# Kernel optimization log

Measured on AMD Instinct MI355X. Metric: run time of the kernel, lower is better.

Reference implementation:

```python
import jax, jax.numpy as jnp
import numpy as np

N = 2048      # total nodes across all graphs
G = 16        # number of graphs
IN = 16       # input_dim
D = 256       # hidden_dim (d_model)
NH = 8        # num_heads
HD = D // NH  # head_dim
FF = 4 * D    # dim_feedforward
L = 4         # num_layers
LAT = 32      # latent_dim
BH = D // 2   # beta_head hidden
LN_EPS = 1e-5


def setup_inputs() -> dict:
    key = jax.random.key(0)
    ks = jax.random.split(key, 32)

    def w(k, shape, fan_in):
        return jax.random.normal(k, shape, jnp.float32) * (1.0 / np.sqrt(fan_in))

    inp = {
        "x": jax.random.normal(ks[0], (N, IN), jnp.float32),
        "coords": jax.random.normal(ks[1], (N, 3), jnp.float32),
        "batch": jnp.sort(jax.random.randint(ks[2], (N,), 0, G)).astype(jnp.int32),
        # input projection
        "Wi": w(ks[3], (IN, D), IN), "bi": jnp.zeros((D,), jnp.float32),
        # per-layer transformer params, stacked on leading layer dim
        "qkv_w": w(ks[4], (L, D, 3 * D), D), "qkv_b": jnp.zeros((L, 3 * D), jnp.float32),
        "out_w": w(ks[5], (L, D, D), D),     "out_b": jnp.zeros((L, D), jnp.float32),
        "ff1_w": w(ks[6], (L, D, FF), D),    "ff1_b": jnp.zeros((L, FF), jnp.float32),
        "ff2_w": w(ks[7], (L, FF, D), FF),   "ff2_b": jnp.zeros((L, D), jnp.float32),
        "ln1_s": jnp.ones((L, D), jnp.float32), "ln1_b": jnp.zeros((L, D), jnp.float32),
        "ln2_s": jnp.ones((L, D), jnp.float32), "ln2_b": jnp.zeros((L, D), jnp.float32),
        # heads
        "lat_w": w(ks[8], (D, LAT), D), "lat_b": jnp.zeros((LAT,), jnp.float32),
        "b1_w": w(ks[9], (D, BH), D),   "b1_b": jnp.zeros((BH,), jnp.float32),
        "b2_w": w(ks[10], (BH, 1), BH), "b2_b": jnp.zeros((1,), jnp.float32),
    }
    return inp


def _layer_norm(h, s, b):
    m = jnp.mean(h, axis=-1, keepdims=True)
    v = jnp.mean(jnp.square(h - m), axis=-1, keepdims=True)
    return (h - m) * jax.lax.rsqrt(v + LN_EPS) * s + b


def _forward(x, batch, Wi, bi, qkv_w, qkv_b, out_w, out_b, ff1_w, ff1_b,
             ff2_w, ff2_b, ln1_s, ln1_b, ln2_s, ln2_b, lat_w, lat_b,
             b1_w, b1_b, b2_w, b2_b):
    n = x.shape[0]
    h = x @ Wi + bi  # [N, D]
    # the per-graph python loop in torch == block-diagonal attention mask
    attn_bias = jnp.where(batch[:, None] == batch[None, :], 0.0, -1e9).astype(h.dtype)  # [N, N]
    scale = 1.0 / np.sqrt(HD)
    for l in range(L):
        qkv = h @ qkv_w[l] + qkv_b[l]                 # [N, 3D]
        q, k, v = jnp.split(qkv, 3, axis=-1)
        q = q.reshape(n, NH, HD)
        k = k.reshape(n, NH, HD)
        v = v.reshape(n, NH, HD)
        scores = jnp.einsum('nhd,mhd->hnm', q, k) * scale + attn_bias[None]  # [H, N, N]
        a = jax.nn.softmax(scores, axis=-1)
        o = jnp.einsum('hnm,mhd->nhd', a, v).reshape(n, D)
        o = o @ out_w[l] + out_b[l]
        h = _layer_norm(h + o, ln1_s[l], ln1_b[l])     # post-norm (torch default)
        f = jax.nn.relu(h @ ff1_w[l] + ff1_b[l]) @ ff2_w[l] + ff2_b[l]
        h = _layer_norm(h + f, ln2_s[l], ln2_b[l])
    lat = h @ lat_w + lat_b                            # [N, LAT]
    norm = jnp.maximum(jnp.linalg.norm(lat, axis=-1, keepdims=True), 1e-12)
    lat = lat / norm * np.sqrt(LAT)
    beta = jax.nn.sigmoid(jax.nn.relu(h @ b1_w + b1_b) @ b2_w + b2_b)  # [N, 1]
    beta = jnp.clip(beta, 1e-6, 1.0 - 1e-6)
    return beta, lat


def reference(x, coords, batch, Wi, bi, qkv_w, qkv_b, out_w, out_b,
              ff1_w, ff1_b, ff2_w, ff2_b, ln1_s, ln1_b, ln2_s, ln2_b,
              lat_w, lat_b, b1_w, b1_b, b2_w, b2_b):
    # coords is accepted (signature fidelity) but unused in the original forward
    del coords
    return _forward(x, batch, Wi, bi, qkv_w, qkv_b, out_w, out_b, ff1_w, ff1_b,
                    ff2_w, ff2_b, ln1_s, ln1_b, ln2_s, ln2_b, lat_w, lat_b,
                    b1_w, b1_b, b2_w, b2_b)
```

## Files before the change

### kernel.cpp

```cpp
#include <hip/hip_runtime.h>
#include <hip/hip_bf16.h>

typedef __attribute__((ext_vector_type(8))) short bf16x8;
typedef __attribute__((ext_vector_type(4))) float f32x4;

__device__ inline float wave_sum64(float v) {
#pragma unroll
  for (int m = 32; m >= 1; m >>= 1) v += __shfl_xor(v, m, 64);
  return v;
}
__device__ inline ushort f2bf(float f) {
  uint u = __float_as_uint(f);
  return (ushort)((u + 0x7FFFu + ((u >> 16) & 1u)) >> 16);
}

__global__ __launch_bounds__(256) void pack_weights(
    const float* __restrict__ qkv_w, const float* __restrict__ out_w,
    const float* __restrict__ ff1_w, const float* __restrict__ ff2_w,
    const float* __restrict__ b1_w, const float* __restrict__ lat_w,
    short* __restrict__ qkv_t, short* __restrict__ out_t,
    short* __restrict__ ff1_t, short* __restrict__ ff2_t,
    short* __restrict__ b1_t, short* __restrict__ lat_t,
    const int* __restrict__ batch, int* __restrict__ starts, int* __restrict__ meta) {
  int t = blockIdx.x;
  if (t == 3112) {
    for (int i = threadIdx.x; i < 2048; i += 256) {
      int b = batch[i];
      if (i == 0) {
        for (int g = 0; g <= b; ++g) starts[g] = 0;
      } else {
        int bp = batch[i - 1];
        for (int g = bp + 1; g <= b; ++g) starts[g] = i;
      }
      if (i == 2047) {
        for (int g = b + 1; g <= 16; ++g) starts[g] = 2048;
      }
    }
    __syncthreads();
    if (threadIdx.x == 0) {
      int nt = 0;
      for (int g = 0; g < 16; ++g) {
        const int js = starts[g], je = starts[g + 1];
        for (int q0 = js; q0 < je; q0 += 16) {
          meta[1 + nt * 3] = q0;
          meta[2 + nt * 3] = js;
          meta[3 + nt * 3] = je;
          ++nt;
        }
      }
      meta[0] = nt;
    }
    return;
  }
  const float* src;
  short* dst;
  int Kd, Nd, rem;
  if (t < 768) {
    int l = t / 192; rem = t % 192; Kd = 256; Nd = 768;
    src = qkv_w + (size_t)l * Kd * Nd; dst = qkv_t + (size_t)l * Nd * Kd;
  } else if (t < 1024) {
    t -= 768; int l = t / 64; rem = t % 64; Kd = 256; Nd = 256;
    src = out_w + (size_t)l * Kd * Nd; dst = out_t + (size_t)l * Nd * Kd;
  } else if (t < 2048) {
    t -= 1024; int l = t / 256; rem = t % 256; Kd = 256; Nd = 1024;
    src = ff1_w + (size_t)l * Kd * Nd; dst = ff1_t + (size_t)l * Nd * Kd;
  } else if (t < 3072) {
    t -= 2048; int l = t / 256; rem = t % 256; Kd = 1024; Nd = 256;
    src = ff2_w + (size_t)l * Kd * Nd; dst = ff2_t + (size_t)l * Nd * Kd;
  } else if (t < 3104) {
    rem = t - 3072; Kd = 256; Nd = 128; src = b1_w; dst = b1_t;
  } else {
    rem = t - 3104; Kd = 256; Nd = 32; src = lat_w; dst = lat_t;
  }
  const int ntn = Nd / 32;
  const int kt = rem / ntn, nt = rem % ntn;

  __shared__ float tile[32][33];
  const int tx = threadIdx.x & 31, ty = threadIdx.x >> 5;
#pragma unroll
  for (int r = 0; r < 4; ++r) {
    int k = kt * 32 + ty + r * 8;
    tile[ty + r * 8][tx] = src[(size_t)k * Nd + nt * 32 + tx];
  }
  __syncthreads();
#pragma unroll
  for (int r = 0; r < 4; ++r) {
    int n = nt * 32 + ty + r * 8;
    dst[(size_t)n * Kd + kt * 32 + tx] = (short)f2bf(tile[tx][ty + r * 8]);
  }
}

__global__ __launch_bounds__(256) void inproj_kernel(
    const float* __restrict__ x, const float* __restrict__ Wi,
    const float* __restrict__ bi, float* __restrict__ h, short* __restrict__ hb) {
  __shared__ float xs[16];
  const int i = blockIdx.x, j = threadIdx.x;
  if (j < 16) xs[j] = x[(size_t)i * 16 + j];
  __syncthreads();
  float acc = bi[j];
#pragma unroll
  for (int k = 0; k < 16; ++k) acc += xs[k] * Wi[k * 256 + j];
  h[(size_t)i * 256 + j] = acc;
  hb[(size_t)i * 256 + j] = (short)f2bf(acc);
}

template <int ACT, int OUTBF, int VT>
__global__ __launch_bounds__(256) void gemm_bf16(
    const short* __restrict__ A, const short* __restrict__ Bt,
    const float* __restrict__ bias, float* __restrict__ Cf, short* __restrict__ Cb,
    short* __restrict__ vtg, int M, int N, int K, int kpb) {
  __shared__ short As[64 * 128];
  __shared__ short Bs[64 * 128];

  const int t = threadIdx.x;
  const int bm = blockIdx.y, bn = blockIdx.x, bz = blockIdx.z;
  const int srow = t >> 2, sq = t & 3;
  const int lane = t & 63, wid = t >> 6;
  const int wr = wid >> 1, wc = wid & 1;
  const int fr = lane & 15, fs = lane >> 4;
  const int rx = srow & 7;

  f32x4 acc[2][2];
#pragma unroll
  for (int m = 0; m < 2; ++m)
#pragma unroll
    for (int n = 0; n < 2; ++n) acc[m][n] = (f32x4){0.f, 0.f, 0.f, 0.f};

  const int kbase = bz * kpb;
  const short* ap = A + (size_t)(bm * 64 + srow) * K + kbase;
  const int ng = bn * 64 + srow;
  const short* bp = Bt + (size_t)ng * K + kbase;

  const int ar0 = wr * 32 + fr, ar1 = ar0 + 16;
  const int bc0 = wc * 32 + fr, bc1 = bc0 + 16;

  for (int k0 = 0; k0 < kpb; k0 += 128) {
    bf16x8 av[4], bv[4];
#pragma unroll
    for (int i = 0; i < 4; ++i) av[i] = *(const bf16x8*)(ap + k0 + (sq * 4 + i) * 8);
    if (ng < N) {
#pragma unroll
      for (int i = 0; i < 4; ++i) bv[i] = *(const bf16x8*)(bp + k0 + (sq * 4 + i) * 8);
    } else {
#pragma unroll
      for (int i = 0; i < 4; ++i) bv[i] = (bf16x8){0, 0, 0, 0, 0, 0, 0, 0};
    }
    __syncthreads();
#pragma unroll
    for (int i = 0; i < 4; ++i) {
      const int s = sq * 4 + i;
      *(bf16x8*)(As + srow * 128 + ((s ^ rx) * 8)) = av[i];
      *(bf16x8*)(Bs + srow * 128 + ((s ^ rx) * 8)) = bv[i];
    }
    __syncthreads();

#pragma unroll
    for (int ks = 0; ks < 4; ++ks) {
      const int u = ks * 4 + fs;
      bf16x8 a0 = *(const bf16x8*)(As + ar0 * 128 + ((u ^ (ar0 & 7)) * 8));
      bf16x8 a1 = *(const bf16x8*)(As + ar1 * 128 + ((u ^ (ar1 & 7)) * 8));
      bf16x8 b0 = *(const bf16x8*)(Bs + bc0 * 128 + ((u ^ (bc0 & 7)) * 8));
      bf16x8 b1 = *(const bf16x8*)(Bs + bc1 * 128 + ((u ^ (bc1 & 7)) * 8));
      acc[0][0] = __builtin_amdgcn_mfma_f32_16x16x32_bf16(a0, b0, acc[0][0], 0, 0, 0);
      acc[0][1] = __builtin_amdgcn_mfma_f32_16x16x32_bf16(a0, b1, acc[0][1], 0, 0, 0);
      acc[1][0] = __builtin_amdgcn_mfma_f32_16x16x32_bf16(a1, b0, acc[1][0], 0, 0, 0);
      acc[1][1] = __builtin_amdgcn_mfma_f32_16x16x32_bf16(a1, b1, acc[1][1], 0, 0, 0);
    }
  }

#pragma unroll
  for (int n = 0; n < 2; ++n) {
    const int col = bn * 64 + wc * 32 + n * 16 + fr;
    if (col >= N) continue;
    const float bvv = (bz == 0) ? bias[col] : 0.f;
#pragma unroll
    for (int m = 0; m < 2; ++m) {
      const int rbase = bm * 64 + wr * 32 + m * 16 + fs * 4;
#pragma unroll
      for (int j = 0; j < 4; ++j) {
        float v = acc[m][n][j] + bvv;
        if (ACT == 1) v = fmaxf(v, 0.f);
        if (OUTBF) {
          const short bfv = (short)f2bf(v);
          Cb[(size_t)(rbase + j) * N + col] = bfv;
          if (VT && col >= 512) {
            vtg[(size_t)(col - 512) * 2048 + rbase + j] = bfv;
          }
        } else {
          Cf[(size_t)(bz * M + rbase + j) * N + col] = v;
        }
      }
    }
  }
}

__global__ __launch_bounds__(256) void attn_direct(
    const short* __restrict__ qkv, const short* __restrict__ vtg,
    const int* __restrict__ meta, short* __restrict__ out) {
  const int wid = blockIdx.x * 4 + (threadIdx.x >> 6);
  const int tile = wid >> 3, h = wid & 7;
  if (tile >= meta[0]) return;
  const int lane = threadIdx.x & 63;
  const int fr = lane & 15, fs = lane >> 4;
  const int q0 = meta[1 + tile * 3];
  const int js = meta[2 + tile * 3];
  const int je = meta[3 + tile * 3];
  const int jbase = js & ~15;
  const int njt = (je - jbase + 15) >> 4;
  const float scale = 0.17677669529663687f;

  const int qrow = min(q0 + fr, 2047);
  const bf16x8 qf = *(const bf16x8*)(qkv + (size_t)qrow * 768 + h * 32 + fs * 8);
  const int jeq = (q0 + fr < je) ? je : 0;

  f32x4 s[16];
#pragma unroll
  for (int jt = 0; jt < 16; ++jt)
    s[jt] = (f32x4){-3.0e38f, -3.0e38f, -3.0e38f, -3.0e38f};

#pragma unroll
  for (int jt = 0; jt < 16; ++jt) {
    if (jt < njt) {
      const int krow = min(jbase + jt * 16 + fr, 2047);
      const bf16x8 kf = *(const bf16x8*)(qkv + (size_t)krow * 768 + 256 + h * 32 + fs * 8);
      s[jt] = __builtin_amdgcn_mfma_f32_16x16x32_bf16(
          kf, qf, (f32x4){0.f, 0.f, 0.f, 0.f}, 0, 0, 0);
    }
  }
  float mx = -3.0e38f;
#pragma unroll
  for (int jt = 0; jt < 16; ++jt) {
    if (jt < njt) {
#pragma unroll
      for (int jj = 0; jj < 4; ++jj) {
        const int j = jbase + jt * 16 + fs * 4 + jj;
        const bool valid = (j >= js) && (j < jeq);
        s[jt][jj] = valid ? s[jt][jj] * scale : -3.0e38f;
        mx = fmaxf(mx, s[jt][jj]);
      }
    }
  }
  mx = fmaxf(mx, __shfl_xor(mx, 16, 64));
  mx = fmaxf(mx, __shfl_xor(mx, 32, 64));
  float l = 0.f;
#pragma unroll
  for (int jt = 0; jt < 16; ++jt) {
#pragma unroll
    for (int jj = 0; jj < 4; ++jj) {
      const float p = __expf(s[jt][jj] - mx);
      s[jt][jj] = p;
      l += p;
    }
  }
  l += __shfl_xor(l, 16, 64);
  l += __shfl_xor(l, 32, 64);

  f32x4 oa[2];
  oa[0] = (f32x4){0.f, 0.f, 0.f, 0.f};
  oa[1] = (f32x4){0.f, 0.f, 0.f, 0.f};
#pragma unroll
  for (int p2 = 0; p2 < 8; ++p2) {
    if (p2 * 2 < njt) {
      bf16x8 pa;
      pa[0] = (short)f2bf(s[p2 * 2][0]);     pa[1] = (short)f2bf(s[p2 * 2][1]);
      pa[2] = (short)f2bf(s[p2 * 2][2]);     pa[3] = (short)f2bf(s[p2 * 2][3]);
      pa[4] = (short)f2bf(s[p2 * 2 + 1][0]); pa[5] = (short)f2bf(s[p2 * 2 + 1][1]);
      pa[6] = (short)f2bf(s[p2 * 2 + 1][2]); pa[7] = (short)f2bf(s[p2 * 2 + 1][3]);
      const int jb0 = min(jbase + p2 * 32 + fs * 4, 2044);
      const int jb1 = min(jbase + p2 * 32 + 16 + fs * 4, 2044);
#pragma unroll
      for (int nt = 0; nt < 2; ++nt) {
        const short* vrow = vtg + (size_t)(h * 32 + nt * 16 + fr) * 2048;
        const short4 v0 = *(const short4*)(vrow + jb0);
        const short4 v1 = *(const short4*)(vrow + jb1);
        bf16x8 vf;
        vf[0] = v0.x; vf[1] = v0.y; vf[2] = v0.z; vf[3] = v0.w;
        vf[4] = v1.x; vf[5] = v1.y; vf[6] = v1.z; vf[7] = v1.w;
        oa[nt] = __builtin_amdgcn_mfma_f32_16x16x32_bf16(pa, vf, oa[nt], 0, 0, 0);
      }
    }
  }

#pragma unroll
  for (int jj = 0; jj < 4; ++jj) {
    const float lq = __shfl(l, fs * 4 + jj, 64);
    const int node = q0 + fs * 4 + jj;
    if (node < je) {
      const float inv = 1.f / lq;
      out[(size_t)node * 256 + h * 32 + fr] = (short)f2bf(oa[0][jj] * inv);
      out[(size_t)node * 256 + h * 32 + 16 + fr] = (short)f2bf(oa[1][jj] * inv);
    }
  }
}

template <int P>
__global__ __launch_bounds__(256) void ln_kernel(
    const float* __restrict__ base, const float* __restrict__ delta,
    const float* __restrict__ s, const float* __restrict__ b,
    float* __restrict__ outf, short* __restrict__ outb) {
  const int row = blockIdx.x * 4 + (threadIdx.x >> 6);
  const int lane = threadIdx.x & 63;
  const float4 xa = *(const float4*)(base + (size_t)row * 256 + lane * 4);
  float4 v = xa;
#pragma unroll
  for (int p = 0; p < P; ++p) {
    const float4 xb = *(const float4*)(delta + (size_t)(p * 2048 + row) * 256 + lane * 4);
    v.x += xb.x; v.y += xb.y; v.z += xb.z; v.w += xb.w;
  }
  float sum = v.x + v.y + v.z + v.w;
  sum = wave_sum64(sum);
  const float mean = sum * (1.f / 256.f);
  float4 d = make_float4(v.x - mean, v.y - mean, v.z - mean, v.w - mean);
  float sq = d.x * d.x + d.y * d.y + d.z * d.z + d.w * d.w;
  sq = wave_sum64(sq);
  const float rs = rsqrtf(sq * (1.f / 256.f) + 1e-5f);
  const float4 sv = *(const float4*)(s + lane * 4);
  const float4 bv = *(const float4*)(b + lane * 4);
  float4 o = make_float4(d.x * rs * sv.x + bv.x, d.y * rs * sv.y + bv.y,
                         d.z * rs * sv.z + bv.z, d.w * rs * sv.w + bv.w);
  *(float4*)(outf + (size_t)row * 256 + lane * 4) = o;
  short4 ob;
  ob.x = (short)f2bf(o.x); ob.y = (short)f2bf(o.y);
  ob.z = (short)f2bf(o.z); ob.w = (short)f2bf(o.w);
  *(short4*)(outb + (size_t)row * 256 + lane * 4) = ob;
}

__global__ __launch_bounds__(256) void lat_kernel(
    const short* __restrict__ A, const short* __restrict__ Bt,
    const float* __restrict__ bias, float* __restrict__ out) {
  __shared__ short As[64 * 128];
  __shared__ short Bs[64 * 128];
  const int t = threadIdx.x;
  const int bm = blockIdx.x;
  const int srow = t >> 2, sq = t & 3;
  const int lane = t & 63, w = t >> 6;
  const int fr = lane & 15, fs = lane >> 4;
  const int rx = srow & 7;

  f32x4 acc[2];
  acc[0] = (f32x4){0.f, 0.f, 0.f, 0.f};
  acc[1] = (f32x4){0.f, 0.f, 0.f, 0.f};

  const short* ap = A + (size_t)(bm * 64 + srow) * 256;
  const short* bp = Bt + (size_t)srow * 256;
  const int ar = w * 16 + fr;

  for (int k0 = 0; k0 < 256; k0 += 128) {
    bf16x8 av[4], bv[4];
#pragma unroll
    for (int i = 0; i < 4; ++i) av[i] = *(const bf16x8*)(ap + k0 + (sq * 4 + i) * 8);
    if (srow < 32) {
#pragma unroll
      for (int i = 0; i < 4; ++i) bv[i] = *(const bf16x8*)(bp + k0 + (sq * 4 + i) * 8);
    } else {
#pragma unroll
      for (int i = 0; i < 4; ++i) bv[i] = (bf16x8){0, 0, 0, 0, 0, 0, 0, 0};
    }
    __syncthreads();
#pragma unroll
    for (int i = 0; i < 4; ++i) {
      const int s = sq * 4 + i;
      *(bf16x8*)(As + srow * 128 + ((s ^ rx) * 8)) = av[i];
      *(bf16x8*)(Bs + srow * 128 + ((s ^ rx) * 8)) = bv[i];
    }
    __syncthreads();
#pragma unroll
    for (int ks = 0; ks < 4; ++ks) {
      const int u = ks * 4 + fs;
      bf16x8 a0 = *(const bf16x8*)(As + ar * 128 + ((u ^ (ar & 7)) * 8));
      bf16x8 b0 = *(const bf16x8*)(Bs + fr * 128 + ((u ^ (fr & 7)) * 8));
      bf16x8 b1 = *(const bf16x8*)(Bs + (16 + fr) * 128 + ((u ^ ((16 + fr) & 7)) * 8));
      acc[0] = __builtin_amdgcn_mfma_f32_16x16x32_bf16(a0, b0, acc[0], 0, 0, 0);
      acc[1] = __builtin_amdgcn_mfma_f32_16x16x32_bf16(a0, b1, acc[1], 0, 0, 0);
    }
  }

  const float b0v = bias[fr], b1v = bias[16 + fr];
#pragma unroll
  for (int j = 0; j < 4; ++j) {
    const int row = bm * 64 + w * 16 + fs * 4 + j;
    float v0 = acc[0][j] + b0v;
    float v1 = acc[1][j] + b1v;
    float ss = v0 * v0 + v1 * v1;
    ss += __shfl_xor(ss, 1, 64);
    ss += __shfl_xor(ss, 2, 64);
    ss += __shfl_xor(ss, 4, 64);
    ss += __shfl_xor(ss, 8, 64);
    const float inv = 5.656854249492381f / fmaxf(sqrtf(ss), 1e-12f);
    out[(size_t)row * 32 + fr] = v0 * inv;
    out[(size_t)row * 32 + 16 + fr] = v1 * inv;
  }
}

__global__ __launch_bounds__(256) void beta_kernel(
    const float* __restrict__ bh, const float* __restrict__ w,
    const float* __restrict__ b2b, float* __restrict__ beta) {
  const int row = blockIdx.x * 4 + (threadIdx.x >> 6);
  const int lane = threadIdx.x & 63;
  float p = bh[(size_t)row * 128 + lane] * w[lane] +
            bh[(size_t)row * 128 + 64 + lane] * w[64 + lane];
  p = wave_sum64(p);
  if (lane == 0) {
    float x = p + b2b[0];
    float sgm = 1.f / (1.f + __expf(-x));
    sgm = fminf(fmaxf(sgm, 1e-6f), 1.f - 1e-6f);
    beta[row] = sgm;
  }
}

extern "C" void kernel_launch(void* const* d_in, const int* in_sizes, int n_in,
                              void* d_out, int out_size, void* d_ws, size_t ws_size,
                              hipStream_t stream) {
  const int N = 2048, D = 256, FF = 1024, L = 4;

  const float* x     = (const float*)d_in[0];
  const int*   batch = (const int*)d_in[2];
  const float* Wi    = (const float*)d_in[3];
  const float* bi    = (const float*)d_in[4];
  const float* qkv_w = (const float*)d_in[5];
  const float* qkv_b = (const float*)d_in[6];
  const float* out_w = (const float*)d_in[7];
  const float* out_b = (const float*)d_in[8];
  const float* ff1_w = (const float*)d_in[9];
  const float* ff1_b = (const float*)d_in[10];
  const float* ff2_w = (const float*)d_in[11];
  const float* ff2_b = (const float*)d_in[12];
  const float* ln1_s = (const float*)d_in[13];
  const float* ln1_b = (const float*)d_in[14];
  const float* ln2_s = (const float*)d_in[15];
  const float* ln2_b = (const float*)d_in[16];
  const float* lat_w = (const float*)d_in[17];
  const float* lat_b = (const float*)d_in[18];
  const float* b1_w  = (const float*)d_in[19];
  const float* b1_b  = (const float*)d_in[20];
  const float* b2_w  = (const float*)d_in[21];
  const float* b2_b  = (const float*)d_in[22];

  float* ws = (float*)d_ws;
  float* h      = ws;
  float* tmp    = h + (size_t)N * D;
  float* bh     = tmp + (size_t)4 * N * D;
  int*  starts  = (int*)(bh + (size_t)N * 128);
  int*  meta    = starts + 32;
  short* hb     = (short*)(meta + 448);
  short* qkvb   = hb + (size_t)N * D;
  short* attnb  = qkvb + (size_t)N * 3 * D;
  short* ffb    = attnb + (size_t)N * D;
  short* vtg    = ffb + (size_t)N * FF;
  short* qkv_t  = vtg + (size_t)256 * 2048;
  short* out_t  = qkv_t + (size_t)L * 768 * 256;
  short* ff1_t  = out_t + (size_t)L * 256 * 256;
  short* ff2_t  = ff1_t + (size_t)L * 1024 * 256;
  short* b1_t   = ff2_t + (size_t)L * 256 * 1024;
  short* lat_t  = b1_t + (size_t)128 * 256;

  float* beta_out = (float*)d_out;
  float* lat_out  = beta_out + N;

  pack_weights<<<3113, 256, 0, stream>>>(qkv_w, out_w, ff1_w, ff2_w, b1_w, lat_w,
                                         qkv_t, out_t, ff1_t, ff2_t, b1_t, lat_t,
                                         batch, starts, meta);
  inproj_kernel<<<N, 256, 0, stream>>>(x, Wi, bi, h, hb);

  for (int l = 0; l < L; ++l) {
    gemm_bf16<0, 1, 1><<<dim3(12, 32, 1), 256, 0, stream>>>(
        hb, qkv_t + (size_t)l * 768 * 256, qkv_b + (size_t)l * 768,
        nullptr, qkvb, vtg, N, 768, 256, 256);
    attn_direct<<<288, 256, 0, stream>>>(qkvb, vtg, meta, attnb);
    gemm_bf16<0, 0, 0><<<dim3(4, 32, 2), 256, 0, stream>>>(
        attnb, out_t + (size_t)l * 256 * 256, out_b + (size_t)l * 256,
        tmp, nullptr, nullptr, N, 256, 256, 128);
    ln_kernel<2><<<N / 4, 256, 0, stream>>>(h, tmp, ln1_s + (size_t)l * D,
                                            ln1_b + (size_t)l * D, h, hb);
    gemm_bf16<1, 1, 0><<<dim3(16, 32, 1), 256, 0, stream>>>(
        hb, ff1_t + (size_t)l * FF * 256, ff1_b + (size_t)l * FF,
        nullptr, ffb, nullptr, N, FF, 256, 256);
    gemm_bf16<0, 0, 0><<<dim3(4, 32, 4), 256, 0, stream>>>(
        ffb, ff2_t + (size_t)l * 256 * FF, ff2_b + (size_t)l * 256,
        tmp, nullptr, nullptr, N, 256, 1024, 256);
    ln_kernel<4><<<N / 4, 256, 0, stream>>>(h, tmp, ln2_s + (size_t)l * D,
                                            ln2_b + (size_t)l * D, h, hb);
  }

  lat_kernel<<<N / 64, 256, 0, stream>>>(hb, lat_t, lat_b, lat_out);
  gemm_bf16<1, 0, 0><<<dim3(2, 32, 1), 256, 0, stream>>>(
      hb, b1_t, b1_b, bh, nullptr, nullptr, N, 128, 256, 256);
  beta_kernel<<<N / 4, 256, 0, stream>>>(bh, b2_w, b2_b, beta_out);
}
```

Baseline: 220.1 us.

## Fuse out-proj/FF2 GEMMs with residual LayerNorm and beta head, tile V transpose

Replaces the split-K fp32 GEMMs plus separate LayerNorm kernels with a single gemm_ln kernel per sublayer. Each block computes 16 full rows of 256 columns, adds bias and residual, and normalizes in-register with a shared-memory reduction. The beta head's two-stage GEMM and dot product become one fused kernel, and the V transpose write in the QKV GEMM now goes through LDS for coalesced stores. This removes the fp32 partial-sum traffic and several launches per layer. The cost is that gemm_ln runs only 128 blocks with no LDS staging or split-K, so the K=1024 FF2 path may have little parallelism, and variance is now computed as E[x²]−mean².

Result: slower. 320.5 us (+45.6%).

```diff
diff --git a/kernel.cpp b/kernel.cpp
--- a/kernel.cpp
+++ b/kernel.cpp
@@ -4,11 +4,6 @@
 typedef __attribute__((ext_vector_type(8))) short bf16x8;
 typedef __attribute__((ext_vector_type(4))) float f32x4;
 
-__device__ inline float wave_sum64(float v) {
-#pragma unroll
-  for (int m = 32; m >= 1; m >>= 1) v += __shfl_xor(v, m, 64);
-  return v;
-}
 __device__ inline ushort f2bf(float f) {
   uint u = __float_as_uint(f);
   return (ushort)((u + 0x7FFFu + ((u >> 16) & 1u)) >> 16);
@@ -104,16 +99,16 @@
   hb[(size_t)i * 256 + j] = (short)f2bf(acc);
 }
 
-template <int ACT, int OUTBF, int VT>
+template <int ACT, int VT>
 __global__ __launch_bounds__(256) void gemm_bf16(
     const short* __restrict__ A, const short* __restrict__ Bt,
-    const float* __restrict__ bias, float* __restrict__ Cf, short* __restrict__ Cb,
-    short* __restrict__ vtg, int M, int N, int K, int kpb) {
+    const float* __restrict__ bias, short* __restrict__ Cb,
+    short* __restrict__ vtg, int N, int K) {
   __shared__ short As[64 * 128];
   __shared__ short Bs[64 * 128];
 
   const int t = threadIdx.x;
-  const int bm = blockIdx.y, bn = blockIdx.x, bz = blockIdx.z;
+  const int bm = blockIdx.y, bn = blockIdx.x;
   const int srow = t >> 2, sq = t & 3;
   const int lane = t & 63, wid = t >> 6;
   const int wr = wid >> 1, wc = wid & 1;
@@ -126,15 +121,13 @@
 #pragma unroll
     for (int n = 0; n < 2; ++n) acc[m][n] = (f32x4){0.f, 0.f, 0.f, 0.f};
 
-  const int kbase = bz * kpb;
-  const short* ap = A + (size_t)(bm * 64 + srow) * K + kbase;
+  const short* ap = A + (size_t)(bm * 64 + srow) * K;
   const int ng = bn * 64 + srow;
-  const short* bp = Bt + (size_t)ng * K + kbase;
-
+  const short* bp = Bt + (size_t)ng * K;
   const int ar0 = wr * 32 + fr, ar1 = ar0 + 16;
   const int bc0 = wc * 32 + fr, bc1 = bc0 + 16;
 
-  for (int k0 = 0; k0 < kpb; k0 += 128) {
+  for (int k0 = 0; k0 < K; k0 += 128) {
     bf16x8 av[4], bv[4];
 #pragma unroll
     for (int i = 0; i < 4; ++i) av[i] = *(const bf16x8*)(ap + k0 + (sq * 4 + i) * 8);
@@ -153,7 +146,6 @@
       *(bf16x8*)(Bs + srow * 128 + ((s ^ rx) * 8)) = bv[i];
     }
     __syncthreads();
-
 #pragma unroll
     for (int ks = 0; ks < 4; ++ks) {
       const int u = ks * 4 + fs;
@@ -171,25 +163,43 @@
 #pragma unroll
   for (int n = 0; n < 2; ++n) {
     const int col = bn * 64 + wc * 32 + n * 16 + fr;
-    if (col >= N) continue;
-    const float bvv = (bz == 0) ? bias[col] : 0.f;
-#pragma unroll
-    for (int m = 0; m < 2; ++m) {
-      const int rbase = bm * 64 + wr * 32 + m * 16 + fs * 4;
-#pragma unroll
-      for (int j = 0; j < 4; ++j) {
-        float v = acc[m][n][j] + bvv;
-        if (ACT == 1) v = fmaxf(v, 0.f);
-        if (OUTBF) {
-          const short bfv = (short)f2bf(v);
-          Cb[(size_t)(rbase + j) * N + col] = bfv;
-          if (VT && col >= 512) {
-            vtg[(size_t)(col - 512) * 2048 + rbase + j] = bfv;
-          }
-        } else {
-          Cf[(size_t)(bz * M + rbase + j) * N + col] = v;
+    if (col < N) {
+      const float bvv = bias[col];
+#pragma unroll
+      for (int m = 0; m < 2; ++m) {
+        const int rbase = bm * 64 + wr * 32 + m * 16 + fs * 4;
+#pragma unroll
+        for (int j = 0; j < 4; ++j) {
+          float v = acc[m][n][j] + bvv;
+          if (ACT == 1) v = fmaxf(v, 0.f);
+          Cb[(size_t)(rbase + j) * N + col] = (short)f2bf(v);
         }
       }
+    }
+  }
+
+  if (VT && bn >= 8) {
+    short* tr = As;
+    __syncthreads();
+#pragma unroll
+    for (int n = 0; n < 2; ++n) {
+      const int c = wc * 32 + n * 16 + fr;
+      const float bvv = bias[bn * 64 + c];
+#pragma unroll
+      for (int m = 0; m < 2; ++m)
+#pragma unroll
+        for (int j = 0; j < 4; ++j) {
+          const int r = wr * 32 + m * 16 + fs * 4 + j;
+          tr[c * 68 + r] = (short)f2bf(acc[m][n][j] + bvv);
+        }
+    }
+    __syncthreads();
+    const int tx = t & 63, ty = t >> 6;
+    const int d0 = bn * 64 - 512, rb = bm * 64;
+#pragma unroll
+    for (int r = 0; r < 16; ++r) {
+      const int d = ty * 16 + r;
+      vtg[(size_t)(d0 + d) * 2048 + rb + tx] = tr[d * 68 + tx];
     }
   }
 }
@@ -280,7 +290,6 @@
       }
     }
   }
-
 #pragma unroll
   for (int jj = 0; jj < 4; ++jj) {
     const float lq = __shfl(l, fs * 4 + jj, 64);
@@ -293,36 +302,123 @@
   }
 }
 
-template <int P>
-__global__ __launch_bounds__(256) void ln_kernel(
-    const float* __restrict__ base, const float* __restrict__ delta,
-    const float* __restrict__ s, const float* __restrict__ b,
-    float* __restrict__ outf, short* __restrict__ outb) {
-  const int row = blockIdx.x * 4 + (threadIdx.x >> 6);
-  const int lane = threadIdx.x & 63;
-  const float4 xa = *(const float4*)(base + (size_t)row * 256 + lane * 4);
-  float4 v = xa;
-#pragma unroll
-  for (int p = 0; p < P; ++p) {
-    const float4 xb = *(const float4*)(delta + (size_t)(p * 2048 + row) * 256 + lane * 4);
-    v.x += xb.x; v.y += xb.y; v.z += xb.z; v.w += xb.w;
-  }
-  float sum = v.x + v.y + v.z + v.w;
-  sum = wave_sum64(sum);
-  const float mean = sum * (1.f / 256.f);
-  float4 d = make_float4(v.x - mean, v.y - mean, v.z - mean, v.w - mean);
-  float sq = d.x * d.x + d.y * d.y + d.z * d.z + d.w * d.w;
-  sq = wave_sum64(sq);
-  const float rs = rsqrtf(sq * (1.f / 256.f) + 1e-5f);
-  const float4 sv = *(const float4*)(s + lane * 4);
-  const float4 bv = *(const float4*)(b + lane * 4);
-  float4 o = make_float4(d.x * rs * sv.x + bv.x, d.y * rs * sv.y + bv.y,
-                         d.z * rs * sv.z + bv.z, d.w * rs * sv.w + bv.w);
-  *(float4*)(outf + (size_t)row * 256 + lane * 4) = o;
-  short4 ob;
-  ob.x = (short)f2bf(o.x); ob.y = (short)f2bf(o.y);
-  ob.z = (short)f2bf(o.z); ob.w = (short)f2bf(o.w);
-  *(short4*)(outb + (size_t)row * 256 + lane * 4) = ob;
+__global__ __launch_bounds__(256) void gemm_ln(
+    const short* __restrict__ A, const short* __restrict__ Bt,
+    const float* __restrict__ bias, const float* __restrict__ lns,
+    const float* __restrict__ lnb, float* __restrict__ hio,
+    short* __restrict__ hbo, int K) {
+  __shared__ float red[128];
+  const int t = threadIdx.x, lane = t & 63, w = t >> 6;
+  const int fr = lane & 15, fs = lane >> 4;
+  const int rb = blockIdx.x * 16;
+
+  f32x4 acc[4];
+#pragma unroll
+  for (int n = 0; n < 4; ++n) acc[n] = (f32x4){0.f, 0.f, 0.f, 0.f};
+  const short* ap = A + (size_t)(rb + fr) * K;
+  const short* bp = Bt + (size_t)(w * 64 + fr) * K;
+  for (int k0 = 0; k0 < K; k0 += 32) {
+    const bf16x8 af = *(const bf16x8*)(ap + k0 + fs * 8);
+#pragma unroll
+    for (int n = 0; n < 4; ++n) {
+      const bf16x8 bf = *(const bf16x8*)(bp + (size_t)n * 16 * K + k0 + fs * 8);
+      acc[n] = __builtin_amdgcn_mfma_f32_16x16x32_bf16(af, bf, acc[n], 0, 0, 0);
+    }
+  }
+
+  float d[4][4];
+#pragma unroll
+  for (int n = 0; n < 4; ++n) {
+    const int col = w * 64 + n * 16 + fr;
+    const float bv = bias[col];
+#pragma unroll
+    for (int j = 0; j < 4; ++j) {
+      const int row = rb + fs * 4 + j;
+      d[n][j] = acc[n][j] + bv + hio[(size_t)row * 256 + col];
+    }
+  }
+  float ps[4], pq[4];
+#pragma unroll
+  for (int j = 0; j < 4; ++j) {
+    ps[j] = d[0][j] + d[1][j] + d[2][j] + d[3][j];
+    pq[j] = d[0][j] * d[0][j] + d[1][j] * d[1][j] + d[2][j] * d[2][j] + d[3][j] * d[3][j];
+#pragma unroll
+    for (int m = 1; m <= 8; m <<= 1) {
+      ps[j] += __shfl_xor(ps[j], m, 64);
+      pq[j] += __shfl_xor(pq[j], m, 64);
+    }
+  }
+  if (fr == 0) {
+#pragma unroll
+    for (int j = 0; j < 4; ++j) {
+      red[w * 16 + fs * 4 + j] = ps[j];
+      red[64 + w * 16 + fs * 4 + j] = pq[j];
+    }
+  }
+  __syncthreads();
+#pragma unroll
+  for (int j = 0; j < 4; ++j) {
+    const int row = fs * 4 + j;
+    const float S = red[row] + red[16 + row] + red[32 + row] + red[48 + row];
+    const float Q = red[64 + row] + red[80 + row] + red[96 + row] + red[112 + row];
+    const float mean = S * (1.f / 256.f);
+    const float var = Q * (1.f / 256.f) - mean * mean;
+    const float rs = rsqrtf(var + 1e-5f);
+#pragma unroll
+    for (int n = 0; n < 4; ++n) {
+      const int col = w * 64 + n * 16 + fr;
+      const float o = (d[n][j] - mean) * rs * lns[col] + lnb[col];
+      hio[(size_t)(rb + row) * 256 + col] = o;
+      hbo[(size_t)(rb + row) * 256 + col] = (short)f2bf(o);
+    }
+  }
+}
+
+__global__ __launch_bounds__(256) void gemm_beta(
+    const short* __restrict__ A, const short* __restrict__ Bt,
+    const float* __restrict__ b1b, const float* __restrict__ w2,
+    const float* __restrict__ b2b, float* __restrict__ beta) {
+  __shared__ float red[64];
+  const int t = threadIdx.x, lane = t & 63, w = t >> 6;
+  const int fr = lane & 15, fs = lane >> 4;
+  const int rb = blockIdx.x * 16;
+
+  f32x4 acc[2];
+  acc[0] = (f32x4){0.f, 0.f, 0.f, 0.f};
+  acc[1] = (f32x4){0.f, 0.f, 0.f, 0.f};
+  const short* ap = A + (size_t)(rb + fr) * 256;
+  const short* bp = Bt + (size_t)(w * 32 + fr) * 256;
+  for (int k0 = 0; k0 < 256; k0 += 32) {
+    const bf16x8 af = *(const bf16x8*)(ap + k0 + fs * 8);
+#pragma unroll
+    for (int n = 0; n < 2; ++n) {
+      const bf16x8 bf = *(const bf16x8*)(bp + (size_t)n * 16 * 256 + k0 + fs * 8);
+      acc[n] = __builtin_amdgcn_mfma_f32_16x16x32_bf16(af, bf, acc[n], 0, 0, 0);
+    }
+  }
+  const int c0 = w * 32 + fr, c1 = c0 + 16;
+  const float b0 = b1b[c0], b1 = b1b[c1];
+  const float w0 = w2[c0], w1 = w2[c1];
+  float part[4];
+#pragma unroll
+  for (int j = 0; j < 4; ++j) {
+    const float d0 = fmaxf(acc[0][j] + b0, 0.f);
+    const float d1 = fmaxf(acc[1][j] + b1, 0.f);
+    part[j] = d0 * w0 + d1 * w1;
+#pragma unroll
+    for (int m = 1; m <= 8; m <<= 1) part[j] += __shfl_xor(part[j], m, 64);
+  }
+  if (fr == 0) {
+#pragma unroll
+    for (int j = 0; j < 4; ++j) red[w * 16 + fs * 4 + j] = part[j];
+  }
+  __syncthreads();
+  if (t < 16) {
+    const float S = red[t] + red[16 + t] + red[32 + t] + red[48 + t] + b2b[0];
+    float sgm = 1.f / (1.f + __expf(-S));
+    sgm = fminf(fmaxf(sgm, 1e-6f), 1.f - 1e-6f);
+    beta[rb + t] = sgm;
+  }
 }
 
 __global__ __launch_bounds__(256) void lat_kernel(
@@ -340,7 +436,6 @@
   f32x4 acc[2];
   acc[0] = (f32x4){0.f, 0.f, 0.f, 0.f};
   acc[1] = (f32x4){0.f, 0.f, 0.f, 0.f};
-
   const short* ap = A + (size_t)(bm * 64 + srow) * 256;
   const short* bp = Bt + (size_t)srow * 256;
   const int ar = w * 16 + fr;
@@ -374,7 +469,6 @@
       acc[1] = __builtin_amdgcn_mfma_f32_16x16x32_bf16(a0, b1, acc[1], 0, 0, 0);
     }
   }
-
   const float b0v = bias[fr], b1v = bias[16 + fr];
 #pragma unroll
   for (int j = 0; j < 4; ++j) {
@@ -389,22 +483,6 @@
     const float inv = 5.656854249492381f / fmaxf(sqrtf(ss), 1e-12f);
     out[(size_t)row * 32 + fr] = v0 * inv;
     out[(size_t)row * 32 + 16 + fr] = v1 * inv;
-  }
-}
-
-__global__ __launch_bounds__(256) void beta_kernel(
-    const float* __restrict__ bh, const float* __restrict__ w,
-    const float* __restrict__ b2b, float* __restrict__ beta) {
-  const int row = blockIdx.x * 4 + (threadIdx.x >> 6);
-  const int lane = threadIdx.x & 63;
-  float p = bh[(size_t)row * 128 + lane] * w[lane] +
-            bh[(size_t)row * 128 + 64 + lane] * w[64 + lane];
-  p = wave_sum64(p);
-  if (lane == 0) {
-    float x = p + b2b[0];
-    float sgm = 1.f / (1.f + __expf(-x));
-    sgm = fminf(fmaxf(sgm, 1e-6f), 1.f - 1e-6f);
-    beta[row] = sgm;
   }
 }
 
@@ -438,9 +516,7 @@
 
   float* ws = (float*)d_ws;
   float* h      = ws;
-  float* tmp    = h + (size_t)N * D;
-  float* bh     = tmp + (size_t)4 * N * D;
-  int*  starts  = (int*)(bh + (size_t)N * 128);
+  int*  starts  = (int*)(h + (size_t)N * D);
   int*  meta    = starts + 32;
   short* hb     = (short*)(meta + 448);
   short* qkvb   = hb + (size_t)N * D;
@@ -463,27 +539,21 @@
   inproj_kernel<<<N, 256, 0, stream>>>(x, Wi, bi, h, hb);
 
   for (int l = 0; l < L; ++l) {
-    gemm_bf16<0, 1, 1><<<dim3(12, 32, 1), 256, 0, stream>>>(
+    gemm_bf16<0, 1><<<dim3(12, 32), 256, 0, stream>>>(
         hb, qkv_t + (size_t)l * 768 * 256, qkv_b + (size_t)l * 768,
-        nullptr, qkvb, vtg, N, 768, 256, 256);
+        qkvb, vtg, 768, 256);
     attn_direct<<<288, 256, 0, stream>>>(qkvb, vtg, meta, attnb);
-    gemm_bf16<0, 0, 0><<<dim3(4, 32, 2), 256, 0, stream>>>(
-        attnb, out_t + (size_t)l * 256 * 256, out_b + (size_t)l * 256,
-        tmp, nullptr, nullptr, N, 256, 256, 128);
-    ln_kernel<2><<<N / 4, 256, 0, stream>>>(h, tmp, ln1_s + (size_t)l * D,
-                                            ln1_b + (size_t)l * D, h, hb);
-    gemm_bf16<1, 1, 0><<<dim3(16, 32, 1), 256, 0, stream>>>(
+    gemm_ln<<<128, 256, 0, stream>>>(attnb, out_t + (size_t)l * 256 * 256,
+                                     out_b + (size_t)l * 256, ln1_s + (size_t)l * D,
+                                     ln1_b + (size_t)l * D, h, hb, 256);
+    gemm_bf16<1, 0><<<dim3(16, 32), 256, 0, stream>>>(
         hb, ff1_t + (size_t)l * FF * 256, ff1_b + (size_t)l * FF,
-        nullptr, ffb, nullptr, N, FF, 256, 256);
-    gemm_bf16<0, 0, 0><<<dim3(4, 32, 4), 256, 0, stream>>>(
-        ffb, ff2_t + (size_t)l * 256 * FF, ff2_b + (size_t)l * 256,
-        tmp, nullptr, nullptr, N, 256, 1024, 256);
-    ln_kernel<4><<<N / 4, 256, 0, stream>>>(h, tmp, ln2_s + (size_t)l * D,
-                                            ln2_b + (size_t)l * D, h, hb);
+        ffb, nullptr, 1024, 256);
+    gemm_ln<<<128, 256, 0, stream>>>(ffb, ff2_t + (size_t)l * 256 * FF,
+                                     ff2_b + (size_t)l * 256, ln2_s + (size_t)l * D,
+                                     ln2_b + (size_t)l * D, h, hb, 1024);
   }
 
   lat_kernel<<<N / 64, 256, 0, stream>>>(hb, lat_t, lat_b, lat_out);
-  gemm_bf16<1, 0, 0><<<dim3(2, 32, 1), 256, 0, stream>>>(
-      hb, b1_t, b1_b, bh, nullptr, nullptr, N, 128, 256, 256);
-  beta_kernel<<<N / 4, 256, 0, stream>>>(bh, b2_w, b2_b, beta_out);
-}
+  gemm_beta<<<128, 256, 0, stream>>>(hb, b1_t, b1_b, b2_w, b2_b, beta_out);
+}
```

## Transpose V through shared memory and fuse beta head GEMM with reduction

Applied to the files above, without the earlier changes.

The QKV GEMM epilogue now stages the V columns in shared memory and writes the transposed V buffer with coalesced row stores, replacing scattered 2-byte strided stores. The beta head's hidden GEMM, ReLU, dot with b2_w and sigmoid are fused into one MFMA kernel, removing the intermediate fp32 buffer and one launch. The transpose adds extra barriers and LDS traffic to V-column blocks. The fused beta kernel reads operands straight from global memory without LDS tiling.

New measurement: 213.6 us. -2.9%, faster.

```diff
diff --git a/kernel.cpp b/kernel.cpp
--- a/kernel.cpp
+++ b/kernel.cpp
@@ -130,7 +130,6 @@
   const short* ap = A + (size_t)(bm * 64 + srow) * K + kbase;
   const int ng = bn * 64 + srow;
   const short* bp = Bt + (size_t)ng * K + kbase;
-
   const int ar0 = wr * 32 + fr, ar1 = ar0 + 16;
   const int bc0 = wc * 32 + fr, bc1 = bc0 + 16;
 
@@ -153,7 +152,6 @@
       *(bf16x8*)(Bs + srow * 128 + ((s ^ rx) * 8)) = bv[i];
     }
     __syncthreads();
-
 #pragma unroll
     for (int ks = 0; ks < 4; ++ks) {
       const int u = ks * 4 + fs;
@@ -171,25 +169,47 @@
 #pragma unroll
   for (int n = 0; n < 2; ++n) {
     const int col = bn * 64 + wc * 32 + n * 16 + fr;
-    if (col >= N) continue;
-    const float bvv = (bz == 0) ? bias[col] : 0.f;
-#pragma unroll
-    for (int m = 0; m < 2; ++m) {
-      const int rbase = bm * 64 + wr * 32 + m * 16 + fs * 4;
-#pragma unroll
-      for (int j = 0; j < 4; ++j) {
-        float v = acc[m][n][j] + bvv;
-        if (ACT == 1) v = fmaxf(v, 0.f);
-        if (OUTBF) {
-          const short bfv = (short)f2bf(v);
-          Cb[(size_t)(rbase + j) * N + col] = bfv;
-          if (VT && col >= 512) {
-            vtg[(size_t)(col - 512) * 2048 + rbase + j] = bfv;
+    if (col < N) {
+      const float bvv = (bz == 0) ? bias[col] : 0.f;
+#pragma unroll
+      for (int m = 0; m < 2; ++m) {
+        const int rbase = bm * 64 + wr * 32 + m * 16 + fs * 4;
+#pragma unroll
+        for (int j = 0; j < 4; ++j) {
+          float v = acc[m][n][j] + bvv;
+          if (ACT == 1) v = fmaxf(v, 0.f);
+          if (OUTBF) {
+            Cb[(size_t)(rbase + j) * N + col] = (short)f2bf(v);
+          } else {
+            Cf[(size_t)(bz * M + rbase + j) * N + col] = v;
           }
-        } else {
-          Cf[(size_t)(bz * M + rbase + j) * N + col] = v;
         }
       }
+    }
+  }
+
+  if (VT && bn >= 8) {
+    short* tr = As;
+    __syncthreads();
+#pragma unroll
+    for (int n = 0; n < 2; ++n) {
+      const int c = wc * 32 + n * 16 + fr;
+      const float bvv = bias[bn * 64 + c];
+#pragma unroll
+      for (int m = 0; m < 2; ++m)
+#pragma unroll
+        for (int j = 0; j < 4; ++j) {
+          const int r = wr * 32 + m * 16 + fs * 4 + j;
+          tr[c * 68 + r] = (short)f2bf(acc[m][n][j] + bvv);
+        }
+    }
+    __syncthreads();
+    const int tx = t & 63, ty = t >> 6;
+    const int d0 = bn * 64 - 512, rb = bm * 64;
+#pragma unroll
+    for (int r = 0; r < 16; ++r) {
+      const int d = ty * 16 + r;
+      vtg[(size_t)(d0 + d) * 2048 + rb + tx] = tr[d * 68 + tx];
     }
   }
 }
@@ -280,7 +300,6 @@
       }
     }
   }
-
 #pragma unroll
   for (int jj = 0; jj < 4; ++jj) {
     const float lq = __shfl(l, fs * 4 + jj, 64);
@@ -307,12 +326,10 @@
     const float4 xb = *(const float4*)(delta + (size_t)(p * 2048 + row) * 256 + lane * 4);
     v.x += xb.x; v.y += xb.y; v.z += xb.z; v.w += xb.w;
   }
-  float sum = v.x + v.y + v.z + v.w;
-  sum = wave_sum64(sum);
+  float sum = wave_sum64(v.x + v.y + v.z + v.w);
   const float mean = sum * (1.f / 256.f);
   float4 d = make_float4(v.x - mean, v.y - mean, v.z - mean, v.w - mean);
-  float sq = d.x * d.x + d.y * d.y + d.z * d.z + d.w * d.w;
-  sq = wave_sum64(sq);
+  float sq = wave_sum64(d.x * d.x + d.y * d.y + d.z * d.z + d.w * d.w);
   const float rs = rsqrtf(sq * (1.f / 256.f) + 1e-5f);
   const float4 sv = *(const float4*)(s + lane * 4);
   const float4 bv = *(const float4*)(b + lane * 4);
@@ -340,7 +357,6 @@
   f32x4 acc[2];
   acc[0] = (f32x4){0.f, 0.f, 0.f, 0.f};
   acc[1] = (f32x4){0.f, 0.f, 0.f, 0.f};
-
   const short* ap = A + (size_t)(bm * 64 + srow) * 256;
   const short* bp = Bt + (size_t)srow * 256;
   const int ar = w * 16 + fr;
@@ -374,7 +390,6 @@
       acc[1] = __builtin_amdgcn_mfma_f32_16x16x32_bf16(a0, b1, acc[1], 0, 0, 0);
     }
   }
-
   const float b0v = bias[fr], b1v = bias[16 + fr];
 #pragma unroll
   for (int j = 0; j < 4; ++j) {
@@ -392,19 +407,50 @@
   }
 }
 
-__global__ __launch_bounds__(256) void beta_kernel(
-    const float* __restrict__ bh, const float* __restrict__ w,
+__global__ __launch_bounds__(256) void gemm_beta(
+    const short* __restrict__ A, const short* __restrict__ Bt,
+    const float* __restrict__ b1b, const float* __restrict__ w2,
     const float* __restrict__ b2b, float* __restrict__ beta) {
-  const int row = blockIdx.x * 4 + (threadIdx.x >> 6);
-  const int lane = threadIdx.x & 63;
-  float p = bh[(size_t)row * 128 + lane] * w[lane] +
-            bh[(size_t)row * 128 + 64 + lane] * w[64 + lane];
-  p = wave_sum64(p);
-  if (lane == 0) {
-    float x = p + b2b[0];
-    float sgm = 1.f / (1.f + __expf(-x));
+  __shared__ float red[64];
+  const int t = threadIdx.x, lane = t & 63, w = t >> 6;
+  const int fr = lane & 15, fs = lane >> 4;
+  const int rb = blockIdx.x * 16;
+
+  f32x4 acc[2];
+  acc[0] = (f32x4){0.f, 0.f, 0.f, 0.f};
+  acc[1] = (f32x4){0.f, 0.f, 0.f, 0.f};
+  const short* ap = A + (size_t)(rb + fr) * 256;
+  const short* bp = Bt + (size_t)(w * 32 + fr) * 256;
+  for (int k0 = 0; k0 < 256; k0 += 32) {
+    const bf16x8 af = *(const bf16x8*)(ap + k0 + fs * 8);
+#pragma unroll
+    for (int n = 0; n < 2; ++n) {
+      const bf16x8 bf = *(const bf16x8*)(bp + (size_t)n * 16 * 256 + k0 + fs * 8);
+      acc[n] = __builtin_amdgcn_mfma_f32_16x16x32_bf16(af, bf, acc[n], 0, 0, 0);
+    }
+  }
+  const int c0 = w * 32 + fr, c1 = c0 + 16;
+  const float b0 = b1b[c0], b1 = b1b[c1];
+  const float w0 = w2[c0], w1 = w2[c1];
+  float part[4];
+#pragma unroll
+  for (int j = 0; j < 4; ++j) {
+    const float d0 = fmaxf(acc[0][j] + b0, 0.f);
+    const float d1 = fmaxf(acc[1][j] + b1, 0.f);
+    part[j] = d0 * w0 + d1 * w1;
+#pragma unroll
+    for (int m = 1; m <= 8; m <<= 1) part[j] += __shfl_xor(part[j], m, 64);
+  }
+  if (fr == 0) {
+#pragma unroll
+    for (int j = 0; j < 4; ++j) red[w * 16 + fs * 4 + j] = part[j];
+  }
+  __syncthreads();
+  if (t < 16) {
+    const float S = red[t] + red[16 + t] + red[32 + t] + red[48 + t] + b2b[0];
+    float sgm = 1.f / (1.f + __expf(-S));
     sgm = fminf(fmaxf(sgm, 1e-6f), 1.f - 1e-6f);
-    beta[row] = sgm;
+    beta[rb + t] = sgm;
   }
 }
 
@@ -439,8 +485,7 @@
   float* ws = (float*)d_ws;
   float* h      = ws;
   float* tmp    = h + (size_t)N * D;
-  float* bh     = tmp + (size_t)4 * N * D;
-  int*  starts  = (int*)(bh + (size_t)N * 128);
+  int*  starts  = (int*)(tmp + (size_t)4 * N * D);
   int*  meta    = starts + 32;
   short* hb     = (short*)(meta + 448);
   short* qkvb   = hb + (size_t)N * D;
@@ -483,7 +528,5 @@
   }
 
   lat_kernel<<<N / 64, 256, 0, stream>>>(hb, lat_t, lat_b, lat_out);
-  gemm_bf16<1, 0, 0><<<dim3(2, 32, 1), 256, 0, stream>>>(
-      hb, b1_t, b1_b, bh, nullptr, nullptr, N, 128, 256, 256);
-  beta_kernel<<<N / 4, 256, 0, stream>>>(bh, b2_w, b2_b, beta_out);
-}
+  gemm_beta<<<128, 256, 0, stream>>>(hb, b1_t, b1_b, b2_w, b2_b, beta_out);
+}
```
